# Kernel optimization log

Measured on AMD Instinct MI355X. Metric: run time of the kernel, lower is better.

The kernel has to match this reference:

```python
import jax, jax.numpy as jnp
import numpy as np
import math

BATCH = 32
F_IN, F_OUT = 16, 32
B_IN, B_OUT = 16, 8
N_SPEC = B_OUT * (4 * B_OUT ** 2 - 1) // 3  # sum_{l<b_out} (2l+1)^2 = 680
ALPHAS = [2.0 * np.pi * a / 6.0 for a in range(6)]
GAMMAS = [2.0 * np.pi * c / 4.0 for c in range(4)]
GRID = [(al, np.pi / 16.0, ga) for al in ALPHAS for ga in GAMMAS]  # 24 (alpha, beta, gamma) points
SCALING = 1.0 / math.sqrt(len(GRID) * F_IN * B_OUT ** 3 / B_IN ** 3)


def _wigner_d(l, beta):
    """Wigner small-d matrix d^l_{m'm}(beta), centered order m',m=-l..l, quantum/Condon-Shortley."""
    lg = math.lgamma
    cb, sb = math.cos(beta / 2.0), math.sin(beta / 2.0)
    d = np.zeros((2 * l + 1, 2 * l + 1))
    for i, mp in enumerate(range(-l, l + 1)):
        for j, m in enumerate(range(-l, l + 1)):
            pref = 0.5 * (lg(l + mp + 1) + lg(l - mp + 1) + lg(l + m + 1) + lg(l - m + 1))
            tot = 0.0
            for s in range(max(0, m - mp), min(l + m, l - mp) + 1):
                den = lg(l + m - s + 1) + lg(s + 1) + lg(mp - m + s + 1) + lg(l - mp - s + 1)
                tot += ((-1.0) ** (mp - m + s) * math.exp(pref - den)
                        * cb ** (2 * l + m - mp - 2 * s) * sb ** (mp - m + 2 * s))
            d[i, j] = tot
    return d


def _quad_weights(b):
    """SOFT quadrature weights at beta_j = pi(2j+1)/(4b); 1/(2b)^2 absorbs the unnormalized 2D FFT."""
    k = np.arange(b)
    j = np.arange(2 * b)
    w = (2.0 / b) * np.sin(np.pi * (2 * j + 1) / (4.0 * b)) * (
        np.sin(np.pi * np.outer(2 * j + 1, 2 * k + 1) / (4.0 * b)) / (2 * k + 1)).sum(axis=1)
    return w / (2 * b) ** 2


def _setup_tables():
    betas_in = np.pi * (2 * np.arange(2 * B_IN) + 1) / (4.0 * B_IN)
    betas_out = np.pi * (2 * np.arange(2 * B_OUT) + 1) / (4.0 * B_OUT)
    w = _quad_weights(B_IN)
    wig_fwd = np.stack([np.concatenate([w[j] * _wigner_d(l, b).ravel() for l in range(B_OUT)])
                        for j, b in enumerate(betas_in)])          # [2*B_IN, N_SPEC]
    wig_inv = np.stack([np.concatenate([(2 * l + 1) * _wigner_d(l, b).ravel() for l in range(B_OUT)])
                        for b in betas_out])                       # [2*B_OUT, N_SPEC]
    F = np.zeros((len(GRID), N_SPEC), dtype=np.complex128)
    for p, (al, be, ga) in enumerate(GRID):
        blocks = []
        for l in range(B_OUT):
            m = np.arange(-l, l + 1)
            D = np.exp(-1j * m[:, None] * al) * _wigner_d(l, be) * np.exp(-1j * m[None, :] * ga)
            blocks.append(np.conj(D).ravel())
        F[p] = np.concatenate(blocks)
    return (wig_fwd.astype(np.float32), wig_inv.astype(np.float32),
            F.real.astype(np.float32), F.imag.astype(np.float32))


def _freq_idx(l, n):
    # packed frequencies -l..-1,0..l with wraparound into an FFT axis of length n
    return np.r_[np.arange(n - l, n), np.arange(l + 1)] if l > 0 else np.arange(1)


def _forward(x, kernel, bias, wigner_fwd, wigner_inv, ft_re, ft_im):
    xf = jnp.fft.fft2(x)  # FFT over (alpha, gamma): [B, Fin, 2b_in, 2b_in, 2b_in] complex64
    # SO3_fft_real: weighted Wigner-d contraction over beta, per degree l
    xhat = []
    for l in range(B_OUT):
        idx = _freq_idx(l, 2 * B_IN)
        xx = xf[:, :, :, idx[:, None], idx[None, :]]  # [B, Fin, beta, 2l+1, 2l+1]
        s0 = l * (4 * l * l - 1) // 3
        wl = wigner_fwd[:, s0:s0 + (2 * l + 1) ** 2].reshape(2 * B_IN, 2 * l + 1, 2 * l + 1)
        xhat.append(jnp.einsum('bmn,zfbmn->mnzf', wl, xx))  # [2l+1, 2l+1, B, Fin]
    # so3_rft of the scaled kernel on the grid: yhat [N_SPEC, Fin, Fout]
    Fc = ft_re + 1j * ft_im  # [P, N_SPEC]
    yhat = jnp.einsum('iop,ps->sio', (kernel * SCALING).astype(jnp.complex64), Fc)
    # so3_mm: per-degree z^l = x^l (y^l)^H, then inverse SO3 FFT
    B = x.shape[0]
    ff = jnp.zeros((B, F_OUT, 2 * B_OUT, 2 * B_OUT, 2 * B_OUT), dtype=xf.dtype)
    for l in range(B_OUT):
        s0 = l * (4 * l * l - 1) // 3
        yl = yhat[s0:s0 + (2 * l + 1) ** 2].reshape(2 * l + 1, 2 * l + 1, F_IN, F_OUT)
        zl = jnp.einsum('mkzf,nkfg->mnzg', xhat[l], jnp.conj(yl))  # [2l+1, 2l+1, B, Fout]
        wl = wigner_inv[:, s0:s0 + (2 * l + 1) ** 2].reshape(2 * B_OUT, 2 * l + 1, 2 * l + 1)
        o = jnp.einsum('mnzg,bmn->zgbmn', zl, wl)  # [B, Fout, beta_out, 2l+1, 2l+1]
        idx = _freq_idx(l, 2 * B_OUT)
        ff = ff.at[:, :, :, idx[:, None], idx[None, :]].add(o)
    out = jnp.real(jnp.fft.ifft2(ff)) * float((2 * B_OUT) ** 2)  # undo ifft 1/N^2, keep real part
    return out + bias


def setup_inputs():
    key = jax.random.key(0)
    k1, k2 = jax.random.split(key)
    x = jax.random.normal(k1, (BATCH, F_IN, 2 * B_IN, 2 * B_IN, 2 * B_IN), dtype=jnp.float32)
    kernel = jax.random.uniform(k2, (F_IN, F_OUT, len(GRID)), minval=-1.0, maxval=1.0, dtype=jnp.float32)
    bias = jnp.zeros((1, F_OUT, 1, 1, 1), jnp.float32)
    wf, wi, fre, fim = _setup_tables()
    return {"x": x, "kernel": kernel, "bias": bias,
            "wigner_fwd": jnp.asarray(wf), "wigner_inv": jnp.asarray(wi),
            "ft_re": jnp.asarray(fre), "ft_im": jnp.asarray(fim)}


def reference(x, kernel, bias, wigner_fwd, wigner_inv, ft_re, ft_im):
    return _forward(x, kernel, bias, wigner_fwd, wigner_inv, ft_re, ft_im)
```

## Files before the change

kernel.cpp:

```cpp
#include <hip/hip_runtime.h>
#include <math.h>


#define NS 680
#define NR 372
#define NP 24
#define NW 15
#define SLB 4
#define SCALING 0.14433756729740643f

__device__ __constant__ int c_s0[9] = {0, 1, 10, 35, 84, 165, 286, 455, 680};
__device__ __constant__ int c_o[9]  = {0, 1, 7, 22, 50, 95, 161, 252, 372};

__device__ __constant__ float2 TW32[32] = {
    { 1.0000000000f,  0.0000000000f}, { 0.9807852804f, -0.1950903220f},
    { 0.9238795325f, -0.3826834324f}, { 0.8314696123f, -0.5555702330f},
    { 0.7071067812f, -0.7071067812f}, { 0.5555702330f, -0.8314696123f},
    { 0.3826834324f, -0.9238795325f}, { 0.1950903220f, -0.9807852804f},
    { 0.0000000000f, -1.0000000000f}, {-0.1950903220f, -0.9807852804f},
    {-0.3826834324f, -0.9238795325f}, {-0.5555702330f, -0.8314696123f},
    {-0.7071067812f, -0.7071067812f}, {-0.8314696123f, -0.5555702330f},
    {-0.9238795325f, -0.3826834324f}, {-0.9807852804f, -0.1950903220f},
    {-1.0000000000f,  0.0000000000f}, {-0.9807852804f,  0.1950903220f},
    {-0.9238795325f,  0.3826834324f}, {-0.8314696123f,  0.5555702330f},
    {-0.7071067812f,  0.7071067812f}, {-0.5555702330f,  0.8314696123f},
    {-0.3826834324f,  0.9238795325f}, {-0.1950903220f,  0.9807852804f},
    { 0.0000000000f,  1.0000000000f}, { 0.1950903220f,  0.9807852804f},
    { 0.3826834324f,  0.9238795325f}, { 0.5555702330f,  0.8314696123f},
    { 0.7071067812f,  0.7071067812f}, { 0.8314696123f,  0.5555702330f},
    { 0.9238795325f,  0.3826834324f}, { 0.9807852804f,  0.1950903220f}};

__device__ __constant__ float2 TW16P[16] = {
    { 1.0000000000f,  0.0000000000f}, { 0.9238795325f,  0.3826834324f},
    { 0.7071067812f,  0.7071067812f}, { 0.3826834324f,  0.9238795325f},
    { 0.0000000000f,  1.0000000000f}, {-0.3826834324f,  0.9238795325f},
    {-0.7071067812f,  0.7071067812f}, {-0.9238795325f,  0.3826834324f},
    {-1.0000000000f,  0.0000000000f}, {-0.9238795325f, -0.3826834324f},
    {-0.7071067812f, -0.7071067812f}, {-0.3826834324f, -0.9238795325f},
    { 0.0000000000f, -1.0000000000f}, { 0.3826834324f, -0.9238795325f},
    { 0.7071067812f, -0.7071067812f}, { 0.9238795325f, -0.3826834324f}};

__global__ __launch_bounds__(256) void A12(const float* __restrict__ x,
                                           float2* __restrict__ xf2) {
    __shared__ __align__(16) float  sx[SLB * 1152];
    __shared__ __align__(16) float2 st[SLB][8][34];
    __shared__ float2 tw[32];
    int blk = blockIdx.x;
    int tid = threadIdx.x;
    if (tid < 32) tw[tid] = TW32[tid];
    {
        const float4* xs = (const float4*)(x + (size_t)blk * (SLB * 1024));
#pragma unroll
        for (int q = 0; q < SLB; q++) {
            int idx = q * 256 + tid;
            float4 v4 = xs[idx];
            int sl = idx >> 8, w = idx & 255;
            *(float4*)&sx[sl * 1152 + (w >> 3) * 36 + (w & 7) * 4] = v4;
        }
    }
    __syncthreads();
    {
        int u = tid >> 3, n = tid & 7;
        float sgn = (n & 1) ? -1.f : 1.f;
        float2 t8[8];
#pragma unroll
        for (int c = 0; c < 8; c++) t8[c] = tw[(n * c) & 31];
        float2 fa1 = tw[(8 * n) & 31];
#pragma unroll
        for (int sl = 0; sl < SLB; sl++) {
            const float* row = &sx[sl * 1152 + u * 36];
            float4 x0 = *(float4*)&row[0],  x1 = *(float4*)&row[4];
            float4 x2 = *(float4*)&row[8],  x3 = *(float4*)&row[12];
            float4 x4 = *(float4*)&row[16], x5 = *(float4*)&row[20];
            float4 x6 = *(float4*)&row[24], x7 = *(float4*)&row[28];
            float y0  = fmaf(sgn, x4.x, x0.x), y1  = fmaf(sgn, x4.y, x0.y);
            float y2  = fmaf(sgn, x4.z, x0.z), y3  = fmaf(sgn, x4.w, x0.w);
            float y4  = fmaf(sgn, x5.x, x1.x), y5  = fmaf(sgn, x5.y, x1.y);
            float y6  = fmaf(sgn, x5.z, x1.z), y7  = fmaf(sgn, x5.w, x1.w);
            float y8  = fmaf(sgn, x6.x, x2.x), y9  = fmaf(sgn, x6.y, x2.y);
            float y10 = fmaf(sgn, x6.z, x2.z), y11 = fmaf(sgn, x6.w, x2.w);
            float y12 = fmaf(sgn, x7.x, x3.x), y13 = fmaf(sgn, x7.y, x3.y);
            float y14 = fmaf(sgn, x7.z, x3.z), y15 = fmaf(sgn, x7.w, x3.w);
            float p0r = y0 * t8[0].x + y1 * t8[1].x + y2 * t8[2].x + y3 * t8[3].x
                      + y4 * t8[4].x + y5 * t8[5].x + y6 * t8[6].x + y7 * t8[7].x;
            float p0i = y0 * t8[0].y + y1 * t8[1].y + y2 * t8[2].y + y3 * t8[3].y
                      + y4 * t8[4].y + y5 * t8[5].y + y6 * t8[6].y + y7 * t8[7].y;
            float p1r = y8 * t8[0].x + y9 * t8[1].x + y10 * t8[2].x + y11 * t8[3].x
                      + y12 * t8[4].x + y13 * t8[5].x + y14 * t8[6].x + y15 * t8[7].x;
            float p1i = y8 * t8[0].y + y9 * t8[1].y + y10 * t8[2].y + y11 * t8[3].y
                      + y12 * t8[4].y + y13 * t8[5].y + y14 * t8[6].y + y15 * t8[7].y;
            float re = p0r + fa1.x * p1r - fa1.y * p1i;
            float im = p0i + fa1.x * p1i + fa1.y * p1r;
            st[sl][n][u] = make_float2(re, im);
        }
    }
    __syncthreads();
    {
        int sl = tid >> 6, m = (tid >> 3) & 7, jj = tid & 7;
        float2 t8[8], fa[4];
#pragma unroll
        for (int c = 0; c < 8; c++) t8[c] = tw[(m * c) & 31];
        fa[0] = make_float2(1.f, 0.f);
#pragma unroll
        for (int a = 1; a < 4; a++) fa[a] = tw[(8 * m * a) & 31];
        float reP = 0.f, imP = 0.f, reN = 0.f, imN = 0.f;
#pragma unroll
        for (int a = 0; a < 4; a++) {
            const float4* spt = (const float4*)&st[sl][jj][a * 8];
            float4 r0 = spt[0], r1 = spt[1], r2 = spt[2], r3 = spt[3];
            float A = r0.x * t8[0].x + r0.z * t8[1].x + r1.x * t8[2].x + r1.z * t8[3].x
                    + r2.x * t8[4].x + r2.z * t8[5].x + r3.x * t8[6].x + r3.z * t8[7].x;
            float B = r0.y * t8[0].y + r0.w * t8[1].y + r1.y * t8[2].y + r1.w * t8[3].y
                    + r2.y * t8[4].y + r2.w * t8[5].y + r3.y * t8[6].y + r3.w * t8[7].y;
            float C = r0.x * t8[0].y + r0.z * t8[1].y + r1.x * t8[2].y + r1.z * t8[3].y
                    + r2.x * t8[4].y + r2.z * t8[5].y + r3.x * t8[6].y + r3.z * t8[7].y;
            float D = r0.y * t8[0].x + r0.w * t8[1].x + r1.y * t8[2].x + r1.w * t8[3].x
                    + r2.y * t8[4].x + r2.w * t8[5].x + r3.y * t8[6].x + r3.w * t8[7].x;
            float prP = A - B, piP = C + D;
            float prN = A + B, piN = C - D;
            reP += fa[a].x * prP - fa[a].y * piP;
            imP += fa[a].x * piP + fa[a].y * prP;
            reN += fa[a].x * prN - fa[a].y * piN;
            imN += fa[a].x * piN + fa[a].y * prN;
        }
        int slice = blk * SLB + sl;
        float2* ob = xf2 + (size_t)slice * 120 + m * 15;
        ob[7 + jj] = make_float2(reP, imP);
        if (jj) ob[7 - jj] = make_float2(reN, imN);
    }
}

__global__ void kP(const float* __restrict__ kern, const float* __restrict__ fre,
                   const float* __restrict__ fim, const float* __restrict__ wf,
                   const float* __restrict__ wi, float2* __restrict__ yhat,
                   float* __restrict__ wfT, float* __restrict__ wiTd) {
    int idx = blockIdx.x * blockDim.x + threadIdx.x;
    if (idx < NS * 512) {
        int s = idx >> 9, fg = idx & 511;
        float re = 0.f, im = 0.f;
        for (int p = 0; p < NP; p++) {
            float kv = kern[fg * NP + p];
            re += kv * fre[p * NS + s];
            im += kv * fim[p * NS + s];
        }
        yhat[(size_t)s * 512 + fg] = make_float2(re * SCALING, im * SCALING);
        return;
    }
    int j = idx - NS * 512;
    if (j < NR * 32) {
        int sp = j >> 5, b = j & 31;
        int l = 0;
#pragma unroll
        for (int t = 1; t < 8; t++) if (sp >= c_o[t]) l = t;
        int K = 2 * l + 1, r = sp - c_o[l];
        int m = r / K, jn = r - m * K;
        int sf = c_s0[l] + (m + l) * K + jn;
        wfT[sp * 32 + b] = wf[b * NS + sf];
        return;
    }
    int k = j - NR * 32;
    if (k >= 16384) return;
    int ni = k & 15, mm = (k >> 4) & 7, b8 = (k >> 7) & 7;
    int l = (k >> 10) & 7, bh = k >> 13;
    int nn = ni - 7;
    float v = 0.f;
    if (ni < 15 && mm <= l && nn >= -l && nn <= l) {
        int K = 2 * l + 1;
        v = wi[(bh * 8 + b8) * NS + c_s0[l] + (mm + l) * K + (nn + l)];
    }
    wiTd[k] = v;
}

__global__ __launch_bounds__(256) void A3(const float2* __restrict__ xf2,
                                          const float* __restrict__ wfT,
                                          float2* __restrict__ xhat) {
    __shared__ float2 sxf[32 * 120];
    int zf = blockIdx.x;
    int tid = threadIdx.x;
    for (int t = tid; t < 32 * 120; t += 256)
        sxf[t] = xf2[(size_t)zf * (32 * 120) + t];
    __syncthreads();
#pragma unroll
    for (int q = 0; q < 2; q++) {
        if (q == 1 && tid >= 116) break;
        int sp = tid + q * 256;
        int l = 0;
#pragma unroll
        for (int t = 1; t < 8; t++) if (sp >= c_o[t]) l = t;
        int K = 2 * l + 1, r = sp - c_o[l];
        int m = r / K, jn = r - m * K;
        int cell = m * 15 + (jn - l + 7);
        const float4* wp = (const float4*)(wfT + sp * 32);
        const float2* xp = sxf + cell;
        float re = 0.f, im = 0.f;
#pragma unroll
        for (int qq = 0; qq < 8; qq++) {
            float4 w4 = wp[qq];
            float2 v0 = xp[(qq * 4 + 0) * 120];
            float2 v1 = xp[(qq * 4 + 1) * 120];
            float2 v2 = xp[(qq * 4 + 2) * 120];
            float2 v3 = xp[(qq * 4 + 3) * 120];
            re += w4.x * v0.x + w4.y * v1.x + w4.z * v2.x + w4.w * v3.x;
            im += w4.x * v0.y + w4.y * v1.y + w4.z * v2.y + w4.w * v3.y;
        }
        xhat[(size_t)sp * 512 + zf] = make_float2(re, im);
    }
}

__global__ __launch_bounds__(256) void kD(const float2* __restrict__ xhat,
                                          const float2* __restrict__ yhat,
                                          float2* __restrict__ zbufT) {
    __shared__ float2 Xs[4][16][18];
    __shared__ float2 Ys[4][16][34];
    int sp = 371 - (blockIdx.x >> 1);
    int zh = blockIdx.x & 1;
    int l = 0;
#pragma unroll
    for (int t = 1; t < 8; t++) if (sp >= c_o[t]) l = t;
    int K = 2 * l + 1, r = sp - c_o[l];
    int m = r / K, jn = r - m * K;
    int sX0 = c_o[l] + m * K;
    int sY0 = c_s0[l] + jn * K;
    int tid = threadIdx.x;
    int zl = tid >> 4;
    int g0 = (tid & 15) * 2;
    float2 acc0 = make_float2(0.f, 0.f), acc1 = make_float2(0.f, 0.f);
    int nchunks = (K + 3) >> 2;
    for (int chunk = 0; chunk < nchunks; ++chunk) {
#pragma unroll
        for (int kw = 0; kw < 4; kw++) {
            int k = chunk * 4 + kw;
            if (k < K)
                Xs[kw][tid & 15][tid >> 4] =
                    xhat[(size_t)(sX0 + k) * 512 + (zh * 16 + (tid >> 4)) * 16 + (tid & 15)];
        }
#pragma unroll
        for (int it = 0; it < 8; it++) {
            int kw = it >> 1;
            int fg = (it & 1) * 256 + tid;
            int k = chunk * 4 + kw;
            if (k < K)
                Ys[kw][fg >> 5][fg & 31] = yhat[(size_t)(sY0 + k) * 512 + fg];
        }
        __syncthreads();
#pragma unroll
        for (int kw = 0; kw < 4; kw++) {
            int k = chunk * 4 + kw;
            if (k < K) {
#pragma unroll
                for (int f = 0; f < 16; f++) {
                    float2 xv  = Xs[kw][f][zl];
                    float2 yv0 = Ys[kw][f][g0];
                    float2 yv1 = Ys[kw][f][g0 + 1];
                    acc0.x += xv.x * yv0.x + xv.y * yv0.y;
                    acc0.y += xv.y * yv0.x - xv.x * yv0.y;
                    acc1.x += xv.x * yv1.x + xv.y * yv1.y;
                    acc1.y += xv.y * yv1.x - xv.x * yv1.y;
                }
            }
        }
        __syncthreads();
    }
    int z0 = zh * 16 + zl;
    zbufT[(size_t)(z0 * 32 + g0) * NR + sp]     = acc0;
    zbufT[(size_t)(z0 * 32 + g0 + 1) * NR + sp] = acc1;
}

__global__ __launch_bounds__(256) void kE4(const float2* __restrict__ zbufT,
                                           const float* __restrict__ wiTd,
                                           const float* __restrict__ bias,
                                           float* __restrict__ out) {
    __shared__ float2 szp[384];
    __shared__ float2 g1[16 * 139];
    __shared__ float2 tw[16];
    int zg = blockIdx.x;
    int g = zg & 31;
    int tid = threadIdx.x;
    if (tid < 16) tw[tid] = TW16P[tid];
    if (tid < 8)    szp[tid] = make_float2(0.f, 0.f);
    if (tid >= 252) szp[tid + 128] = make_float2(0.f, 0.f);
    for (int t = tid; t < NR; t += 256) szp[8 + t] = zbufT[(size_t)zg * NR + t];
    __syncthreads();
    {
        int b = tid & 15, mm = (tid >> 4) & 7, vh = tid >> 7;
        int bh = b >> 3, b8 = b & 7;
        const int co[8] = {0, 1, 7, 22, 50, 95, 161, 252};
        float2 ff[15];
#pragma unroll
        for (int n = 0; n < 15; n++) ff[n] = make_float2(0.f, 0.f);
#pragma unroll
        for (int l = 0; l < 8; l++) {
            const float4* wl = (const float4*)(wiTd + ((((bh * 8 + l) * 8 + b8) * 8 + mm) << 4));
            float4 w0 = wl[0], w1 = wl[1], w2 = wl[2], w3 = wl[3];
            float wreg[16] = {w0.x, w0.y, w0.z, w0.w, w1.x, w1.y, w1.z, w1.w,
                              w2.x, w2.y, w2.z, w2.w, w3.x, w3.y, w3.z, w3.w};
            int sp = 1 + co[l] + mm * (2 * l + 1) + l;
#pragma unroll
            for (int ni = 0; ni < 15; ni++) {
                float w = wreg[ni];
                float2 v = szp[sp + ni];
                ff[ni].x += w * v.x; ff[ni].y += w * v.y;
            }
        }
#pragma unroll
        for (int j = 0; j < 8; j++) {
            int v = vh * 8 + j;
            float re = 0.f, im = 0.f;
#pragma unroll
            for (int n = 0; n < 15; n++) {
                float2 c = tw[((n - 7) * v) & 15];
                float2 a = ff[n];
                re += a.x * c.x - a.y * c.y;
                im += a.x * c.y + a.y * c.x;
            }
            g1[b * 139 + mm * 17 + v] = make_float2(re, im);
        }
    }
    __syncthreads();
    {
        int b = tid & 15, u = tid >> 4;
        float o[16];
#pragma unroll
        for (int j = 0; j < 16; j++) o[j] = g1[b * 139 + j].x;
#pragma unroll
        for (int m = 1; m < 8; m++) {
            float2 c = tw[(m * u) & 15];
#pragma unroll
            for (int j = 0; j < 16; j++) {
                float2 a = g1[b * 139 + m * 17 + j];
                o[j] += 2.f * (a.x * c.x - a.y * c.y);
            }
        }
        float bv = bias[g];
        float* ob = out + ((size_t)zg * 16 + b) * 256 + u * 16;
#pragma unroll
        for (int j = 0; j < 16; j += 4)
            *(float4*)&ob[j] = make_float4(o[j] + bv, o[j + 1] + bv, o[j + 2] + bv, o[j + 3] + bv);
    }
}

extern "C" void kernel_launch(void* const* d_in, const int* in_sizes, int n_in,
                              void* d_out, int out_size, void* d_ws, size_t ws_size,
                              hipStream_t stream) {
    const float* x    = (const float*)d_in[0];
    const float* kern = (const float*)d_in[1];
    const float* bias = (const float*)d_in[2];
    const float* wf   = (const float*)d_in[3];
    const float* wi   = (const float*)d_in[4];
    const float* fre  = (const float*)d_in[5];
    const float* fim  = (const float*)d_in[6];
    float* out = (float*)d_out;

    char* ws = (char*)d_ws;
    float2* xf2   = (float2*)ws;
    float2* xhat  = (float2*)(ws + 15728640);
    float2* yhat  = (float2*)(ws + 17252352);
    float2* zbufT = (float2*)(ws + 20037632);
    float*  wfT   = (float*)(ws + 23085056);
    float*  wiTd  = (float*)(ws + 23132672);

    A12<<<4096, 256, 0, stream>>>(x, xf2);
    kP<<<1471, 256, 0, stream>>>(kern, fre, fim, wf, wi, yhat, wfT, wiTd);
    A3<<<512, 256, 0, stream>>>(xf2, wfT, xhat);
    kD<<<744, 256, 0, stream>>>(xhat, yhat, zbufT);
    kE4<<<1024, 256, 0, stream>>>(zbufT, wiTd, bias, out);
}
```

Before: 87.82 us.

## Fuse Wigner beta-contraction into FFT kernel and merge table-prep with partial reduce

The forward Wigner contraction over beta moves into the 2D-FFT kernel. Each block contracts its 4 beta slices against Wigner weights staged in shared memory and writes 372-entry partial sums, replacing the 120-complex-per-slice FFT output. A new kernel M sums the 8 partials per (batch, feature) into xhat and also builds yhat and the inverse Wigner table, which removes one launch and the large xf2 intermediate. The kD inner loop also reads two adjacent Ys values as one float4. The cost is extra shared memory per block in the FFT kernel, which may lower occupancy.

```diff
diff --git a/kernel.cpp b/kernel.cpp
--- a/kernel.cpp
+++ b/kernel.cpp
@@ -40,13 +40,16 @@
     { 0.0000000000f, -1.0000000000f}, { 0.3826834324f, -0.9238795325f},
     { 0.7071067812f, -0.7071067812f}, { 0.9238795325f, -0.3826834324f}};
 
-__global__ __launch_bounds__(256) void A12(const float* __restrict__ x,
-                                           float2* __restrict__ xf2) {
-    __shared__ __align__(16) float  sx[SLB * 1152];
+__global__ __launch_bounds__(256) void A12W(const float* __restrict__ x,
+                                            const float* __restrict__ wf,
+                                            float2* __restrict__ part) {
+    __shared__ __align__(16) float  sxraw[SLB * 1152];
     __shared__ __align__(16) float2 st[SLB][8][34];
+    __shared__ float swf[4 * NS];
     __shared__ float2 tw[32];
     int blk = blockIdx.x;
     int tid = threadIdx.x;
+    int b0 = (blk & 7) * 4;
     if (tid < 32) tw[tid] = TW32[tid];
     {
         const float4* xs = (const float4*)(x + (size_t)blk * (SLB * 1024));
@@ -55,8 +58,12 @@
             int idx = q * 256 + tid;
             float4 v4 = xs[idx];
             int sl = idx >> 8, w = idx & 255;
-            *(float4*)&sx[sl * 1152 + (w >> 3) * 36 + (w & 7) * 4] = v4;
-        }
+            *(float4*)&sxraw[sl * 1152 + (w >> 3) * 36 + (w & 7) * 4] = v4;
+        }
+    }
+    {
+        const float* wsrc = wf + (size_t)b0 * NS;
+        for (int t = tid; t < 4 * NS; t += 256) swf[t] = wsrc[t];
     }
     __syncthreads();
     {
@@ -68,7 +75,7 @@
         float2 fa1 = tw[(8 * n) & 31];
 #pragma unroll
         for (int sl = 0; sl < SLB; sl++) {
-            const float* row = &sx[sl * 1152 + u * 36];
+            const float* row = &sxraw[sl * 1152 + u * 36];
             float4 x0 = *(float4*)&row[0],  x1 = *(float4*)&row[4];
             float4 x2 = *(float4*)&row[8],  x3 = *(float4*)&row[12];
             float4 x4 = *(float4*)&row[16], x5 = *(float4*)&row[20];
@@ -95,6 +102,7 @@
         }
     }
     __syncthreads();
+    float2* xfb = (float2*)sxraw;
     {
         int sl = tid >> 6, m = (tid >> 3) & 7, jj = tid & 7;
         float2 t8[8], fa[4];
@@ -123,43 +131,78 @@
             reN += fa[a].x * prN - fa[a].y * piN;
             imN += fa[a].x * piN + fa[a].y * prN;
         }
-        int slice = blk * SLB + sl;
-        float2* ob = xf2 + (size_t)slice * 120 + m * 15;
+        float2* ob = xfb + sl * 120 + m * 15;
         ob[7 + jj] = make_float2(reP, imP);
         if (jj) ob[7 - jj] = make_float2(reN, imN);
     }
-}
-
-__global__ void kP(const float* __restrict__ kern, const float* __restrict__ fre,
-                   const float* __restrict__ fim, const float* __restrict__ wf,
-                   const float* __restrict__ wi, float2* __restrict__ yhat,
-                   float* __restrict__ wfT, float* __restrict__ wiTd) {
-    int idx = blockIdx.x * blockDim.x + threadIdx.x;
-    if (idx < NS * 512) {
-        int s = idx >> 9, fg = idx & 511;
+    __syncthreads();
+    {
+#pragma unroll
+        for (int q = 0; q < 2; q++) {
+            if (q == 1 && tid >= NR - 256) break;
+            int sp = tid + q * 256;
+            int l = 0;
+#pragma unroll
+            for (int t = 1; t < 8; t++) if (sp >= c_o[t]) l = t;
+            int K = 2 * l + 1, r = sp - c_o[l];
+            int mrow = r / K, jn = r - mrow * K;
+            int cell = mrow * 15 + (jn - l + 7);
+            int sf = c_s0[l] + (mrow + l) * K + jn;
+            float re = 0.f, im = 0.f;
+#pragma unroll
+            for (int c = 0; c < 4; c++) {
+                float w = swf[c * NS + sf];
+                float2 v = xfb[c * 120 + cell];
+                re += w * v.x; im += w * v.y;
+            }
+            part[(size_t)blk * NR + sp] = make_float2(re, im);
+        }
+    }
+}
+
+__global__ __launch_bounds__(256) void M(const float2* __restrict__ part,
+                                         const float* __restrict__ kern,
+                                         const float* __restrict__ fre,
+                                         const float* __restrict__ fim,
+                                         const float* __restrict__ wi,
+                                         float2* __restrict__ xhat,
+                                         float2* __restrict__ yhat,
+                                         float* __restrict__ wiTd) {
+    __shared__ float2 s[8 * NR];
+    int bid = blockIdx.x, tid = threadIdx.x;
+    if (bid < 512) {
+        int zf = bid;
+        const float2* p = part + (size_t)zf * 8 * NR;
+        for (int t = tid; t < 8 * NR; t += 256) s[t] = p[t];
+        __syncthreads();
+#pragma unroll
+        for (int q = 0; q < 2; q++) {
+            if (q == 1 && tid >= NR - 256) break;
+            int sp = tid + q * 256;
+            float re = 0.f, im = 0.f;
+#pragma unroll
+            for (int c = 0; c < 8; c++) {
+                float2 v = s[c * NR + sp];
+                re += v.x; im += v.y;
+            }
+            xhat[(size_t)sp * 512 + zf] = make_float2(re, im);
+        }
+        return;
+    }
+    int j = bid - 512;
+    if (j < 1360) {
+        int idx = j * 256 + tid;
+        int ss = idx >> 9, fg = idx & 511;
         float re = 0.f, im = 0.f;
         for (int p = 0; p < NP; p++) {
             float kv = kern[fg * NP + p];
-            re += kv * fre[p * NS + s];
-            im += kv * fim[p * NS + s];
-        }
-        yhat[(size_t)s * 512 + fg] = make_float2(re * SCALING, im * SCALING);
+            re += kv * fre[p * NS + ss];
+            im += kv * fim[p * NS + ss];
+        }
+        yhat[(size_t)ss * 512 + fg] = make_float2(re * SCALING, im * SCALING);
         return;
     }
-    int j = idx - NS * 512;
-    if (j < NR * 32) {
-        int sp = j >> 5, b = j & 31;
-        int l = 0;
-#pragma unroll
-        for (int t = 1; t < 8; t++) if (sp >= c_o[t]) l = t;
-        int K = 2 * l + 1, r = sp - c_o[l];
-        int m = r / K, jn = r - m * K;
-        int sf = c_s0[l] + (m + l) * K + jn;
-        wfT[sp * 32 + b] = wf[b * NS + sf];
-        return;
-    }
-    int k = j - NR * 32;
-    if (k >= 16384) return;
+    int k = (j - 1360) * 256 + tid;
     int ni = k & 15, mm = (k >> 4) & 7, b8 = (k >> 7) & 7;
     int l = (k >> 10) & 7, bh = k >> 13;
     int nn = ni - 7;
@@ -171,47 +214,11 @@
     wiTd[k] = v;
 }
 
-__global__ __launch_bounds__(256) void A3(const float2* __restrict__ xf2,
-                                          const float* __restrict__ wfT,
-                                          float2* __restrict__ xhat) {
-    __shared__ float2 sxf[32 * 120];
-    int zf = blockIdx.x;
-    int tid = threadIdx.x;
-    for (int t = tid; t < 32 * 120; t += 256)
-        sxf[t] = xf2[(size_t)zf * (32 * 120) + t];
-    __syncthreads();
-#pragma unroll
-    for (int q = 0; q < 2; q++) {
-        if (q == 1 && tid >= 116) break;
-        int sp = tid + q * 256;
-        int l = 0;
-#pragma unroll
-        for (int t = 1; t < 8; t++) if (sp >= c_o[t]) l = t;
-        int K = 2 * l + 1, r = sp - c_o[l];
-        int m = r / K, jn = r - m * K;
-        int cell = m * 15 + (jn - l + 7);
-        const float4* wp = (const float4*)(wfT + sp * 32);
-        const float2* xp = sxf + cell;
-        float re = 0.f, im = 0.f;
-#pragma unroll
-        for (int qq = 0; qq < 8; qq++) {
-            float4 w4 = wp[qq];
-            float2 v0 = xp[(qq * 4 + 0) * 120];
-            float2 v1 = xp[(qq * 4 + 1) * 120];
-            float2 v2 = xp[(qq * 4 + 2) * 120];
-            float2 v3 = xp[(qq * 4 + 3) * 120];
-            re += w4.x * v0.x + w4.y * v1.x + w4.z * v2.x + w4.w * v3.x;
-            im += w4.x * v0.y + w4.y * v1.y + w4.z * v2.y + w4.w * v3.y;
-        }
-        xhat[(size_t)sp * 512 + zf] = make_float2(re, im);
-    }
-}
-
 __global__ __launch_bounds__(256) void kD(const float2* __restrict__ xhat,
                                           const float2* __restrict__ yhat,
                                           float2* __restrict__ zbufT) {
-    __shared__ float2 Xs[4][16][18];
-    __shared__ float2 Ys[4][16][34];
+    __shared__ __align__(16) float2 Xs[4][16][18];
+    __shared__ __align__(16) float2 Ys[4][16][34];
     int sp = 371 - (blockIdx.x >> 1);
     int zh = blockIdx.x & 1;
     int l = 0;
@@ -250,12 +257,11 @@
 #pragma unroll
                 for (int f = 0; f < 16; f++) {
                     float2 xv  = Xs[kw][f][zl];
-                    float2 yv0 = Ys[kw][f][g0];
-                    float2 yv1 = Ys[kw][f][g0 + 1];
-                    acc0.x += xv.x * yv0.x + xv.y * yv0.y;
-                    acc0.y += xv.y * yv0.x - xv.x * yv0.y;
-                    acc1.x += xv.x * yv1.x + xv.y * yv1.y;
-                    acc1.y += xv.y * yv1.x - xv.x * yv1.y;
+                    float4 y4  = *(const float4*)&Ys[kw][f][g0];
+                    acc0.x += xv.x * y4.x + xv.y * y4.y;
+                    acc0.y += xv.y * y4.x - xv.x * y4.y;
+                    acc1.x += xv.x * y4.z + xv.y * y4.w;
+                    acc1.y += xv.y * y4.z - xv.x * y4.w;
                 }
             }
         }
@@ -352,16 +358,14 @@
     float* out = (float*)d_out;
 
     char* ws = (char*)d_ws;
-    float2* xf2   = (float2*)ws;
-    float2* xhat  = (float2*)(ws + 15728640);
-    float2* yhat  = (float2*)(ws + 17252352);
-    float2* zbufT = (float2*)(ws + 20037632);
-    float*  wfT   = (float*)(ws + 23085056);
-    float*  wiTd  = (float*)(ws + 23132672);
-
-    A12<<<4096, 256, 0, stream>>>(x, xf2);
-    kP<<<1471, 256, 0, stream>>>(kern, fre, fim, wf, wi, yhat, wfT, wiTd);
-    A3<<<512, 256, 0, stream>>>(xf2, wfT, xhat);
+    float2* part  = (float2*)ws;
+    float2* xhat  = (float2*)(ws + 12189696);
+    float2* yhat  = (float2*)(ws + 13713408);
+    float2* zbufT = (float2*)(ws + 16498688);
+    float*  wiTd  = (float*)(ws + 19546112);
+
+    A12W<<<4096, 256, 0, stream>>>(x, wf, part);
+    M<<<1936, 256, 0, stream>>>(part, kern, fre, fim, wi, xhat, yhat, wiTd);
     kD<<<744, 256, 0, stream>>>(xhat, yhat, zbufT);
     kE4<<<1024, 256, 0, stream>>>(zbufT, wiTd, bias, out);
 }
```

New measurement: 90.09 us. 2.6% more time.
